# Kernel tuning notes

Hardware: AMD Instinct MI355X
Metric: run time of the kernel (lower is better)

The kernel has to match this reference:

```python
import jax, jax.numpy as jnp
import numpy as np

NUM_EMBEDDINGS = 4096
EMBEDDING_DIM = 256


def setup_inputs() -> dict:
    key = jax.random.key(0)
    k1, k2 = jax.random.split(key)
    # x: [B, C, H, W] latent feature map, C == embedding_dim
    x = jax.random.normal(k1, (4, EMBEDDING_DIM, 64, 64), dtype=jnp.float32)
    # codebook initialized uniform(-1/K, 1/K) as in the torch module
    emb = jax.random.uniform(
        k2, (NUM_EMBEDDINGS, EMBEDDING_DIM), dtype=jnp.float32,
        minval=-1.0 / NUM_EMBEDDINGS, maxval=1.0 / NUM_EMBEDDINGS)
    return {"x": x, "emb": emb}


def reference(x, emb):
    # x: [B, C, H, W] -> x_flat: [B, L, C] with L = H*W
    B, C = x.shape[0], x.shape[1]
    x_flat = x.reshape(B, C, -1).transpose(0, 2, 1)
    x_sq = jnp.sum(x_flat * x_flat, axis=2, keepdims=True)      # [B, L, 1]
    e_sq = jnp.sum(emb * emb, axis=1)                            # [K]
    dots = jnp.einsum('blc,kc->blk', x_flat, emb)                # [B, L, K]
    distances = x_sq + e_sq - 2.0 * dots
    closest_indices = jnp.argmin(distances, axis=2)              # [B, L]
    return closest_indices, distances
```

## Files before the change

### kernel.cpp

```cpp
#include <hip/hip_runtime.h>
#include <hip/hip_fp16.h>

#define BB 4
#define CC 256
#define LL 4096
#define MM 16384
#define KK 4096
#define MARGIN 1.0e-4f

typedef _Float16 half8 __attribute__((ext_vector_type(8)));
typedef _Float16 half4_ __attribute__((ext_vector_type(4)));
typedef float f32x4 __attribute__((ext_vector_type(4)));

#define GLOAD16(gp, lp) __builtin_amdgcn_global_load_lds( \
    (const __attribute__((address_space(1))) void*)(gp),  \
    (__attribute__((address_space(3))) void*)(lp), 16, 0, 0)

__global__ void vq_prep(const float* __restrict__ x, const float* __restrict__ emb,
                        _Float16* __restrict__ xh, float* __restrict__ xsq,
                        _Float16* __restrict__ eh, float* __restrict__ esq) {
  __shared__ float tl[32][260];
  const int t = threadIdx.x;
  if (blockIdx.x < 512) {
    const int b = blockIdx.x >> 7, l0 = (blockIdx.x & 127) * 32;
    const float* src = x + (size_t)b * CC * LL + l0;
#pragma unroll
    for (int it = 0; it < 32; ++it) {
      const int idx = it * 256 + t;
      const int c = idx >> 5, l = idx & 31;
      tl[l][c] = src[(size_t)c * LL + l];
    }
    __syncthreads();
#pragma unroll
    for (int it = 0; it < 4; ++it) {
      const int u = it * 256 + t;
      const int l = u >> 5, c8 = (u & 31) * 8;
      half8 h;
#pragma unroll
      for (int j = 0; j < 8; ++j) h[j] = (_Float16)tl[l][c8 + j];
      *(half8*)(xh + ((size_t)(b * LL + l0 + l)) * CC + c8) = h;
    }
    if (t < 32) {
      float S[2];
#pragma unroll
      for (int blk = 0; blk < 2; ++blk) {
        float v[16];
#pragma unroll
        for (int ln = 0; ln < 16; ++ln) {
          float q[8];
#pragma unroll
          for (int j = 0; j < 8; ++j) {
            const float xv = tl[t][blk * 128 + j * 16 + ln];
            q[j] = xv * xv;
          }
          v[ln] = ((q[0] + q[1]) + (q[2] + q[3])) + ((q[4] + q[5]) + (q[6] + q[7]));
        }
        float s1[8], s2[4], s3[2];
#pragma unroll
        for (int ln = 0; ln < 8; ++ln) s1[ln] = v[ln] + v[ln + 8];
#pragma unroll
        for (int ln = 0; ln < 4; ++ln) s2[ln] = s1[ln] + s1[ln + 4];
#pragma unroll
        for (int ln = 0; ln < 2; ++ln) s3[ln] = s2[ln] + s2[ln + 2];
        S[blk] = s3[0] + s3[1];
      }
      xsq[b * LL + l0 + t] = S[0] + S[1];
    }
  } else {
    const int lane = t & 63, w = t >> 6;
    const int q = (blockIdx.x - 512) * 4 + w;
    const float4 v = ((const float4*)(emb + (size_t)q * CC))[lane];
    float vv[4] = {v.x, v.y, v.z, v.w};
    _Float16 h[4];
#pragma unroll
    for (int i = 0; i < 4; ++i) h[i] = (_Float16)(vv[i] * 4096.0f);
    *(half4_*)(eh + (size_t)q * CC + lane * 4) = half4_{h[0], h[1], h[2], h[3]};
    if (lane == 0) {
      const float* pe = emb + (size_t)q * CC;
      float S[2];
#pragma unroll
      for (int blk = 0; blk < 2; ++blk) {
        float vt[16];
#pragma unroll
        for (int ln = 0; ln < 16; ++ln) {
          float qq[8];
#pragma unroll
          for (int j = 0; j < 8; ++j) {
            const float ev = pe[blk * 128 + j * 16 + ln];
            qq[j] = ev * ev;
          }
          vt[ln] = ((qq[0] + qq[1]) + (qq[2] + qq[3])) + ((qq[4] + qq[5]) + (qq[6] + qq[7]));
        }
        float s1[8], s2[4], s3[2];
#pragma unroll
        for (int ln = 0; ln < 8; ++ln) s1[ln] = vt[ln] + vt[ln + 8];
#pragma unroll
        for (int ln = 0; ln < 4; ++ln) s2[ln] = s1[ln] + s1[ln + 4];
#pragma unroll
        for (int ln = 0; ln < 2; ++ln) s3[ln] = s2[ln] + s2[ln + 2];
        S[blk] = s3[0] + s3[1];
      }
      esq[q] = S[0] + S[1];
    }
  }
}

__global__ __launch_bounds__(256) void vq_gemm(
    const _Float16* __restrict__ xh, const _Float16* __restrict__ eh,
    const float* __restrict__ xsq, const float* __restrict__ esq,
    float* __restrict__ out,
    float* __restrict__ ps1, int* __restrict__ pi1, float* __restrict__ ps2) {
  __shared__ __align__(16) char smem[49152];
  float* sOut = (float*)smem;

  const int t = threadIdx.x, lane = t & 63, wid = t >> 6;
  const int wm = wid >> 1, wn = wid & 1;
  const int m0 = blockIdx.x * 128, n0 = blockIdx.y * 128;
  const int lm = lane & 15, kb = lane >> 4;

  const int srow = lane >> 2;
  const int scol = (lane & 3) * 8;
  const int chunk0 = wid * 2, chunk1 = wid * 2 + 1;
  const int row0 = chunk0 * 16 + srow, row1 = chunk1 * 16 + srow;

  float ev[4], xs4[4][4];
#pragma unroll
  for (int ni = 0; ni < 4; ++ni) ev[ni] = esq[n0 + wn * 64 + ni * 16 + lm];
#pragma unroll
  for (int mi = 0; mi < 4; ++mi)
#pragma unroll
    for (int r = 0; r < 4; ++r)
      xs4[mi][r] = xsq[m0 + wm * 64 + mi * 16 + kb * 4 + r];
  __builtin_amdgcn_sched_barrier(0);

#define SA(b) ((_Float16*)(smem + (b) * 16384))
#define SB(b) ((_Float16*)(smem + (b) * 16384 + 8192))
#define STAGE(ks, buf) do {                                                   \
    const int kc_ = (ks) * 32 + scol;                                         \
    GLOAD16(xh + (size_t)(m0 + row0) * CC + kc_, SA(buf) + chunk0 * 512);     \
    GLOAD16(eh + (size_t)(n0 + row0) * CC + kc_, SB(buf) + chunk0 * 512);     \
    GLOAD16(xh + (size_t)(m0 + row1) * CC + kc_, SA(buf) + chunk1 * 512);     \
    GLOAD16(eh + (size_t)(n0 + row1) * CC + kc_, SB(buf) + chunk1 * 512);     \
  } while (0)

  f32x4 acc[4][4] = {};
  STAGE(0, 0);
  STAGE(1, 1);
#pragma unroll
  for (int ks = 0; ks < 8; ++ks) {
    const int cur = ks % 3;
    if (ks < 6) {
      STAGE(ks + 2, (ks + 2) % 3);
      asm volatile("s_waitcnt vmcnt(8)" ::: "memory");
    } else if (ks == 6) {
      asm volatile("s_waitcnt vmcnt(4)" ::: "memory");
    } else {
      asm volatile("s_waitcnt vmcnt(0)" ::: "memory");
    }
    __builtin_amdgcn_s_barrier();
    __builtin_amdgcn_sched_barrier(0);

    half8 a[4], bfr[4];
#pragma unroll
    for (int i = 0; i < 4; ++i) {
      a[i]   = *(const half8*)&SA(cur)[(wm * 64 + i * 16 + lm) * 32 + kb * 8];
      bfr[i] = *(const half8*)&SB(cur)[(wn * 64 + i * 16 + lm) * 32 + kb * 8];
    }
#pragma unroll
    for (int mi = 0; mi < 4; ++mi)
#pragma unroll
      for (int ni = 0; ni < 4; ++ni)
        acc[mi][ni] = __builtin_amdgcn_mfma_f32_16x16x32_f16(a[mi], bfr[ni], acc[mi][ni], 0, 0, 0);

    if (ks < 7) {
      asm volatile("s_waitcnt lgkmcnt(0)" ::: "memory");
      __builtin_amdgcn_s_barrier();
      __builtin_amdgcn_sched_barrier(0);
    }
  }
#undef STAGE

#define EPI_BAR() do {                                          \
    asm volatile("s_waitcnt lgkmcnt(0)" ::: "memory");          \
    __builtin_amdgcn_s_barrier();                               \
    __builtin_amdgcn_sched_barrier(0);                          \
  } while (0)

  const int swz = kb << 4;
  const int erow = t >> 3, ej = t & 7;
  const int esw = ((erow >> 2) & 3) << 4;
  const int egm0 = m0 + (erow >> 4) * 64 + (erow & 15);

#pragma unroll
  for (int mi = 0; mi < 4; ++mi) {
#pragma unroll
    for (int r = 0; r < 4; ++r) {
      const int row = wm * 16 + kb * 4 + r;
#pragma unroll
      for (int ni = 0; ni < 4; ++ni) {
        float t1 = xs4[mi][r] + ev[ni];
        float d = t1 - acc[mi][ni][r] * 4.8828125e-4f;
        sOut[row * 128 + ((wn * 64 + ni * 16 + lm) ^ swz)] = d;
      }
    }
    EPI_BAR();
    float s1 = 3.4e38f, s2 = 3.4e38f;
    int q1 = 0x7fffffff;
    const int gm = egm0 + mi * 16;
#pragma unroll
    for (int i = 0; i < 4; ++i) {
      const int c = 4 * ej + 32 * i;
      const f32x4 v = *(const f32x4*)&sOut[erow * 128 + (c ^ esw)];
      __builtin_nontemporal_store(v, (f32x4*)(out + MM + (size_t)gm * (size_t)KK + n0 + c));
#pragma unroll
      for (int e = 0; e < 4; ++e) {
        const float d = v[e];
        const int q = n0 + c + e;
        if (d < s1 || (d == s1 && q < q1)) { s2 = s1; s1 = d; q1 = q; }
        else s2 = fminf(s2, d);
      }
    }
#pragma unroll
    for (int off = 1; off < 8; off <<= 1) {
      float o1 = __shfl_xor(s1, off), o2 = __shfl_xor(s2, off);
      int oq = __shfl_xor(q1, off);
      float mx = fmaxf(s1, o1);
      if (o1 < s1 || (o1 == s1 && oq < q1)) { s1 = o1; q1 = oq; }
      s2 = fminf(fminf(s2, o2), mx);
    }
    if (ej == 0) {
      const size_t pidx = (size_t)gm * 32 + blockIdx.y;
      ps1[pidx] = s1; pi1[pidx] = q1; ps2[pidx] = s2;
    }
    if (mi < 3) EPI_BAR();
  }
#undef EPI_BAR
#undef SA
#undef SB
}

__global__ void vq_finish(const float* __restrict__ ps1, const int* __restrict__ pi1,
                          const float* __restrict__ ps2, const float* __restrict__ dist,
                          const float* __restrict__ x, const float* __restrict__ emb,
                          const float* __restrict__ xsq, const float* __restrict__ esq,
                          float* __restrict__ out) {
  __shared__ float xr[4][CC];
  __shared__ int cq[4][64];
  __shared__ int cnt[4];
  const int lane = threadIdx.x & 63, w = threadIdx.x >> 6;
  const int m = blockIdx.x * 4 + w;

  float s1 = 3.4e38f, s2 = 3.4e38f;
  int q1 = 0x7fffffff;
  if (lane < 32) {
    const size_t base = (size_t)m * 32 + lane;
    s1 = ps1[base]; s2 = ps2[base]; q1 = pi1[base];
  }
#pragma unroll
  for (int off = 1; off < 32; off <<= 1) {
    float o1 = __shfl_xor(s1, off), o2 = __shfl_xor(s2, off);
    int oq = __shfl_xor(q1, off);
    float mx = fmaxf(s1, o1);
    if (o1 < s1 || (o1 == s1 && oq < q1)) { s1 = o1; q1 = oq; }
    s2 = fminf(fminf(s2, o2), mx);
  }
  s1 = __shfl(s1, 0); s2 = __shfl(s2, 0); q1 = __shfl(q1, 0);

  if (s2 - s1 > MARGIN) {
    if (lane == 0) out[m] = (float)q1;
    return;
  }

  const int b = m >> 12, l = m & 4095;
#pragma unroll
  for (int j = 0; j < 4; ++j)
    xr[w][lane * 4 + j] = x[((size_t)b * CC + lane * 4 + j) * LL + l];
  if (lane == 0) cnt[w] = 0;

  const float thr = s1 + MARGIN;
  const float4* d4 = (const float4*)(dist + (size_t)m * KK);
  for (int i = 0; i < 16; ++i) {
    float4 v = d4[i * 64 + lane];
    float vv[4] = {v.x, v.y, v.z, v.w};
#pragma unroll
    for (int e = 0; e < 4; ++e)
      if (vv[e] <= thr) {
        int slot = atomicAdd(&cnt[w], 1);
        if (slot < 64) cq[w][slot] = (i * 64 + lane) * 4 + e;
      }
  }
  const int nc = min(cnt[w], 64);
  float bs = 3.4e38f;
  int bq = 0x7fffffff;
  if (lane < nc) {
    const int q = cq[w][lane];
    const float* e = emb + (size_t)q * CC;
    float a = 0.f;
    for (int c = 0; c < CC; ++c) a = fmaf(xr[w][c], e[c], a);
    float t1 = xsq[m] + esq[q];
    bs = t1 - 2.0f * a;
    bq = q;
  }
#pragma unroll
  for (int off = 1; off < 64; off <<= 1) {
    float os = __shfl_xor(bs, off);
    int oq = __shfl_xor(bq, off);
    if (os < bs || (os == bs && oq < bq)) { bs = os; bq = oq; }
  }
  if (lane == 0) out[m] = (float)bq;
}

extern "C" void kernel_launch(void* const* d_in, const int* in_sizes, int n_in,
                              void* d_out, int out_size, void* d_ws, size_t ws_size,
                              hipStream_t stream) {
  const float* x = (const float*)d_in[0];
  const float* emb = (const float*)d_in[1];
  float* out = (float*)d_out;
  char* ws = (char*)d_ws;

  _Float16* xh = (_Float16*)(ws + 0);
  _Float16* eh = (_Float16*)(ws + 8388608);
  float* xsq = (float*)(ws + 10485760);
  float* esq = (float*)(ws + 10551296);
  float* ps1 = (float*)(ws + 10567680);
  int*   pi1 = (int*)(ws + 12664832);
  float* ps2 = (float*)(ws + 14761984);

  vq_prep<<<1536, 256, 0, stream>>>(x, emb, xh, xsq, eh, esq);
  vq_gemm<<<dim3(128, 32), 256, 0, stream>>>(xh, eh, xsq, esq, out, ps1, pi1, ps2);
  vq_finish<<<4096, 256, 0, stream>>>(ps1, pi1, ps2, out + MM, x, emb, xsq, esq, out);
}
```

Before: 127.9 us.

## Shrink GEMM tile to 64x64 single-wave blocks and drop block barriers

Each GEMM workgroup becomes one 64-lane wave computing a 64x64 tile instead of four waves on a 128x128 tile. LDS staging, the epilogue transpose and the per-row min reductions no longer need workgroup barriers, and the finish kernel now reduces 64 partials per row. The aim is to remove barrier stalls and raise occupancy. The cost is double the global loads of fp16 inputs per output, twice the partial-min traffic, and four times as many blocks.

```diff
diff --git a/kernel.cpp b/kernel.cpp
--- a/kernel.cpp
+++ b/kernel.cpp
@@ -105,42 +105,42 @@
   }
 }
 
-__global__ __launch_bounds__(256) void vq_gemm(
+__global__ __launch_bounds__(64) void vq_gemm(
     const _Float16* __restrict__ xh, const _Float16* __restrict__ eh,
     const float* __restrict__ xsq, const float* __restrict__ esq,
     float* __restrict__ out,
     float* __restrict__ ps1, int* __restrict__ pi1, float* __restrict__ ps2) {
-  __shared__ __align__(16) char smem[49152];
+  __shared__ __align__(16) char smem[24576];
   float* sOut = (float*)smem;
 
-  const int t = threadIdx.x, lane = t & 63, wid = t >> 6;
-  const int wm = wid >> 1, wn = wid & 1;
-  const int m0 = blockIdx.x * 128, n0 = blockIdx.y * 128;
+  const int lane = threadIdx.x;
+  const int m0 = blockIdx.x * 64, n0 = blockIdx.y * 64;
   const int lm = lane & 15, kb = lane >> 4;
-
   const int srow = lane >> 2;
   const int scol = (lane & 3) * 8;
-  const int chunk0 = wid * 2, chunk1 = wid * 2 + 1;
-  const int row0 = chunk0 * 16 + srow, row1 = chunk1 * 16 + srow;
 
   float ev[4], xs4[4][4];
 #pragma unroll
-  for (int ni = 0; ni < 4; ++ni) ev[ni] = esq[n0 + wn * 64 + ni * 16 + lm];
+  for (int ni = 0; ni < 4; ++ni) ev[ni] = esq[n0 + ni * 16 + lm];
 #pragma unroll
   for (int mi = 0; mi < 4; ++mi)
 #pragma unroll
     for (int r = 0; r < 4; ++r)
-      xs4[mi][r] = xsq[m0 + wm * 64 + mi * 16 + kb * 4 + r];
+      xs4[mi][r] = xsq[m0 + mi * 16 + kb * 4 + r];
   __builtin_amdgcn_sched_barrier(0);
 
-#define SA(b) ((_Float16*)(smem + (b) * 16384))
-#define SB(b) ((_Float16*)(smem + (b) * 16384 + 8192))
+#define SA(b) ((_Float16*)(smem + (b) * 8192))
+#define SB(b) ((_Float16*)(smem + (b) * 8192 + 4096))
 #define STAGE(ks, buf) do {                                                   \
     const int kc_ = (ks) * 32 + scol;                                         \
-    GLOAD16(xh + (size_t)(m0 + row0) * CC + kc_, SA(buf) + chunk0 * 512);     \
-    GLOAD16(eh + (size_t)(n0 + row0) * CC + kc_, SB(buf) + chunk0 * 512);     \
-    GLOAD16(xh + (size_t)(m0 + row1) * CC + kc_, SA(buf) + chunk1 * 512);     \
-    GLOAD16(eh + (size_t)(n0 + row1) * CC + kc_, SB(buf) + chunk1 * 512);     \
+    GLOAD16(xh + (size_t)(m0 +  0 + srow) * CC + kc_, SA(buf) + 0 * 512);     \
+    GLOAD16(xh + (size_t)(m0 + 16 + srow) * CC + kc_, SA(buf) + 1 * 512);     \
+    GLOAD16(xh + (size_t)(m0 + 32 + srow) * CC + kc_, SA(buf) + 2 * 512);     \
+    GLOAD16(xh + (size_t)(m0 + 48 + srow) * CC + kc_, SA(buf) + 3 * 512);     \
+    GLOAD16(eh + (size_t)(n0 +  0 + srow) * CC + kc_, SB(buf) + 0 * 512);     \
+    GLOAD16(eh + (size_t)(n0 + 16 + srow) * CC + kc_, SB(buf) + 1 * 512);     \
+    GLOAD16(eh + (size_t)(n0 + 32 + srow) * CC + kc_, SB(buf) + 2 * 512);     \
+    GLOAD16(eh + (size_t)(n0 + 48 + srow) * CC + kc_, SB(buf) + 3 * 512);     \
   } while (0)
 
   f32x4 acc[4][4] = {};
@@ -150,91 +150,79 @@
   for (int ks = 0; ks < 8; ++ks) {
     const int cur = ks % 3;
     if (ks < 6) {
+      asm volatile("s_waitcnt lgkmcnt(0)" ::: "memory");
+      __builtin_amdgcn_sched_barrier(0);
       STAGE(ks + 2, (ks + 2) % 3);
+      asm volatile("s_waitcnt vmcnt(16)" ::: "memory");
+    } else if (ks == 6) {
       asm volatile("s_waitcnt vmcnt(8)" ::: "memory");
-    } else if (ks == 6) {
-      asm volatile("s_waitcnt vmcnt(4)" ::: "memory");
     } else {
       asm volatile("s_waitcnt vmcnt(0)" ::: "memory");
     }
-    __builtin_amdgcn_s_barrier();
     __builtin_amdgcn_sched_barrier(0);
 
     half8 a[4], bfr[4];
 #pragma unroll
     for (int i = 0; i < 4; ++i) {
-      a[i]   = *(const half8*)&SA(cur)[(wm * 64 + i * 16 + lm) * 32 + kb * 8];
-      bfr[i] = *(const half8*)&SB(cur)[(wn * 64 + i * 16 + lm) * 32 + kb * 8];
+      a[i]   = *(const half8*)&SA(cur)[(i * 16 + lm) * 32 + kb * 8];
+      bfr[i] = *(const half8*)&SB(cur)[(i * 16 + lm) * 32 + kb * 8];
     }
 #pragma unroll
     for (int mi = 0; mi < 4; ++mi)
 #pragma unroll
       for (int ni = 0; ni < 4; ++ni)
         acc[mi][ni] = __builtin_amdgcn_mfma_f32_16x16x32_f16(a[mi], bfr[ni], acc[mi][ni], 0, 0, 0);
-
-    if (ks < 7) {
-      asm volatile("s_waitcnt lgkmcnt(0)" ::: "memory");
-      __builtin_amdgcn_s_barrier();
-      __builtin_amdgcn_sched_barrier(0);
-    }
   }
 #undef STAGE
 
-#define EPI_BAR() do {                                          \
-    asm volatile("s_waitcnt lgkmcnt(0)" ::: "memory");          \
-    __builtin_amdgcn_s_barrier();                               \
-    __builtin_amdgcn_sched_barrier(0);                          \
-  } while (0)
+  asm volatile("s_waitcnt lgkmcnt(0)" ::: "memory");
+  __builtin_amdgcn_sched_barrier(0);
 
   const int swz = kb << 4;
-  const int erow = t >> 3, ej = t & 7;
-  const int esw = ((erow >> 2) & 3) << 4;
-  const int egm0 = m0 + (erow >> 4) * 64 + (erow & 15);
-
-#pragma unroll
-  for (int mi = 0; mi < 4; ++mi) {
+#pragma unroll
+  for (int mi = 0; mi < 4; ++mi)
 #pragma unroll
     for (int r = 0; r < 4; ++r) {
-      const int row = wm * 16 + kb * 4 + r;
+      const int row = mi * 16 + kb * 4 + r;
 #pragma unroll
       for (int ni = 0; ni < 4; ++ni) {
         float t1 = xs4[mi][r] + ev[ni];
         float d = t1 - acc[mi][ni][r] * 4.8828125e-4f;
-        sOut[row * 128 + ((wn * 64 + ni * 16 + lm) ^ swz)] = d;
+        sOut[row * 64 + ((ni * 16 + lm) ^ swz)] = d;
       }
     }
-    EPI_BAR();
+  asm volatile("s_waitcnt lgkmcnt(0)" ::: "memory");
+  __builtin_amdgcn_sched_barrier(0);
+
+#pragma unroll
+  for (int i = 0; i < 16; ++i) {
+    const int row = i * 4 + (lane >> 4);
+    const int c = (lane & 15) * 4;
+    const f32x4 v = *(const f32x4*)&sOut[row * 64 + (c ^ ((i & 3) << 4))];
+    const int gm = m0 + row;
+    __builtin_nontemporal_store(v, (f32x4*)(out + MM + (size_t)gm * (size_t)KK + n0 + c));
     float s1 = 3.4e38f, s2 = 3.4e38f;
     int q1 = 0x7fffffff;
-    const int gm = egm0 + mi * 16;
-#pragma unroll
-    for (int i = 0; i < 4; ++i) {
-      const int c = 4 * ej + 32 * i;
-      const f32x4 v = *(const f32x4*)&sOut[erow * 128 + (c ^ esw)];
-      __builtin_nontemporal_store(v, (f32x4*)(out + MM + (size_t)gm * (size_t)KK + n0 + c));
-#pragma unroll
-      for (int e = 0; e < 4; ++e) {
-        const float d = v[e];
-        const int q = n0 + c + e;
-        if (d < s1 || (d == s1 && q < q1)) { s2 = s1; s1 = d; q1 = q; }
-        else s2 = fminf(s2, d);
-      }
-    }
-#pragma unroll
-    for (int off = 1; off < 8; off <<= 1) {
+#pragma unroll
+    for (int e = 0; e < 4; ++e) {
+      const float d = v[e];
+      const int q = n0 + c + e;
+      if (d < s1 || (d == s1 && q < q1)) { s2 = s1; s1 = d; q1 = q; }
+      else s2 = fminf(s2, d);
+    }
+#pragma unroll
+    for (int off = 1; off < 16; off <<= 1) {
       float o1 = __shfl_xor(s1, off), o2 = __shfl_xor(s2, off);
       int oq = __shfl_xor(q1, off);
       float mx = fmaxf(s1, o1);
       if (o1 < s1 || (o1 == s1 && oq < q1)) { s1 = o1; q1 = oq; }
       s2 = fminf(fminf(s2, o2), mx);
     }
-    if (ej == 0) {
-      const size_t pidx = (size_t)gm * 32 + blockIdx.y;
+    if ((lane & 15) == 0) {
+      const size_t pidx = (size_t)gm * 64 + blockIdx.y;
       ps1[pidx] = s1; pi1[pidx] = q1; ps2[pidx] = s2;
     }
-    if (mi < 3) EPI_BAR();
-  }
-#undef EPI_BAR
+  }
 #undef SA
 #undef SB
 }
@@ -250,21 +238,17 @@
   const int lane = threadIdx.x & 63, w = threadIdx.x >> 6;
   const int m = blockIdx.x * 4 + w;
 
-  float s1 = 3.4e38f, s2 = 3.4e38f;
-  int q1 = 0x7fffffff;
-  if (lane < 32) {
-    const size_t base = (size_t)m * 32 + lane;
-    s1 = ps1[base]; s2 = ps2[base]; q1 = pi1[base];
-  }
-#pragma unroll
-  for (int off = 1; off < 32; off <<= 1) {
+  const size_t base = (size_t)m * 64 + lane;
+  float s1 = ps1[base], s2 = ps2[base];
+  int q1 = pi1[base];
+#pragma unroll
+  for (int off = 1; off < 64; off <<= 1) {
     float o1 = __shfl_xor(s1, off), o2 = __shfl_xor(s2, off);
     int oq = __shfl_xor(q1, off);
     float mx = fmaxf(s1, o1);
     if (o1 < s1 || (o1 == s1 && oq < q1)) { s1 = o1; q1 = oq; }
     s2 = fminf(fminf(s2, o2), mx);
   }
-  s1 = __shfl(s1, 0); s2 = __shfl(s2, 0); q1 = __shfl(q1, 0);
 
   if (s2 - s1 > MARGIN) {
     if (lane == 0) out[m] = (float)q1;
@@ -323,10 +307,10 @@
   float* xsq = (float*)(ws + 10485760);
   float* esq = (float*)(ws + 10551296);
   float* ps1 = (float*)(ws + 10567680);
-  int*   pi1 = (int*)(ws + 12664832);
-  float* ps2 = (float*)(ws + 14761984);
+  int*   pi1 = (int*)(ws + 14761984);
+  float* ps2 = (float*)(ws + 18956288);
 
   vq_prep<<<1536, 256, 0, stream>>>(x, emb, xh, xsq, eh, esq);
-  vq_gemm<<<dim3(128, 32), 256, 0, stream>>>(xh, eh, xsq, esq, out, ps1, pi1, ps2);
+  vq_gemm<<<dim3(256, 64), 64, 0, stream>>>(xh, eh, xsq, esq, out, ps1, pi1, ps2);
   vq_finish<<<4096, 256, 0, stream>>>(ps1, pi1, ps2, out + MM, x, emb, xsq, esq, out);
 }
```

Measured after the change: 214.1 us. 1.67x slower.
